# Kernel tuning notes

Hardware: AMD Instinct MI355X
Metric: run time of the kernel (lower is better)

Reference implementation:

```python
import jax, jax.numpy as jnp
import numpy as np

EMBED = 1024
DFF = 4096


def _layernorm(x, g, b, eps=1e-5):
    mu = jnp.mean(x, axis=-1, keepdims=True)
    var = jnp.var(x, axis=-1, keepdims=True)
    return (x - mu) * jax.lax.rsqrt(var + eps) * g + b


def setup_inputs() -> dict:
    key = jax.random.key(0)
    ks = jax.random.split(key, 14)
    s = 1.0 / np.sqrt(EMBED)
    sf = 1.0 / np.sqrt(DFF)
    d = {
        "src": jax.random.normal(ks[0], (4, 2048, EMBED), dtype=jnp.float32),
        "Wq": jax.random.uniform(ks[1], (EMBED, EMBED), jnp.float32, -s, s),
        "bq": jnp.zeros((EMBED,), jnp.float32),
        "Wk": jax.random.uniform(ks[2], (EMBED, EMBED), jnp.float32, -s, s),
        "bk": jnp.zeros((EMBED,), jnp.float32),
        "Wv": jax.random.uniform(ks[3], (EMBED, EMBED), jnp.float32, -s, s),
        "bv": jnp.zeros((EMBED,), jnp.float32),
        "Wo": jax.random.uniform(ks[4], (EMBED, EMBED), jnp.float32, -s, s),
        "bo": jnp.zeros((EMBED,), jnp.float32),
        "W1": jax.random.uniform(ks[5], (EMBED, DFF), jnp.float32, -s, s),
        "b1": jnp.zeros((DFF,), jnp.float32),
        "W2": jax.random.uniform(ks[6], (DFF, EMBED), jnp.float32, -sf, sf),
        "b2": jnp.zeros((EMBED,), jnp.float32),
        "g1": jnp.ones((EMBED,), jnp.float32),
        "be1": jnp.zeros((EMBED,), jnp.float32),
        "g2": jnp.ones((EMBED,), jnp.float32),
        "be2": jnp.zeros((EMBED,), jnp.float32),
    }
    return d


def reference(src, Wq, bq, Wk, bk, Wv, bv, Wo, bo, W1, b1, W2, b2, g1, be1, g2, be2):
    # Q/K/V projections: [b, s, d]
    Q = src @ Wq + bq
    K = src @ Wk + bk
    V = src @ Wv + bv
    # Single-head, UNSCALED attention (faithful to source: no 1/sqrt(d), num_heads unused)
    scores = jnp.einsum("bqd,bkd->bqk", Q, K)  # [b, s, s]
    weights = jax.nn.softmax(scores, axis=-1)
    attn = jnp.einsum("bqk,bkd->bqd", weights, V)
    attn = attn @ Wo + bo
    x = _layernorm(src + attn, g1, be1)
    ff = jax.nn.relu(x @ W1 + b1) @ W2 + b2
    return _layernorm(x + ff, g2, be2)
```

## Files before the change

### kernel.cpp

```cpp
#include <hip/hip_runtime.h>
#include <stdint.h>

typedef unsigned short u16;
typedef _Float16 v8h __attribute__((ext_vector_type(8)));
typedef float v4f __attribute__((ext_vector_type(4)));

static __device__ __forceinline__ float h2f(u16 u) {
    union { u16 s; _Float16 h; } v; v.s = u; return (float)v.h;
}
static __device__ __forceinline__ u16 f2h(float f) {
    union { u16 s; _Float16 h; } v; v.h = (_Float16)f; return v.s;
}

static __device__ __forceinline__ void gload_lds16(const u16* g, const u16* l) {
    __builtin_amdgcn_global_load_lds(
        (const __attribute__((address_space(1))) uint32_t*)(uintptr_t)g,
        (__attribute__((address_space(3))) uint32_t*)(uintptr_t)l,
        16, 0, 0);
}

__global__ __launch_bounds__(256) void cvt_f16(const float* __restrict__ in,
                                               u16* __restrict__ out, int n8) {
    const int i = blockIdx.x * 256 + threadIdx.x;
    if (i >= n8) return;
    const float4 a = ((const float4*)in)[2 * i];
    const float4 b = ((const float4*)in)[2 * i + 1];
    u16 o[8] = {f2h(a.x), f2h(a.y), f2h(a.z), f2h(a.w),
                f2h(b.x), f2h(b.y), f2h(b.z), f2h(b.w)};
    *(uint4*)(out + (size_t)i * 8) = *(const uint4*)o;
}

__global__ __launch_bounds__(256) void transpose_all(
    const float* __restrict__ Wq, const float* __restrict__ Wk,
    const float* __restrict__ Wv, const float* __restrict__ Wo,
    const float* __restrict__ W1, const float* __restrict__ W2,
    u16* __restrict__ WqkvT, u16* __restrict__ WoT,
    u16* __restrict__ W1T, u16* __restrict__ W2T)
{
    int t = blockIdx.x;
    const float* in; u16* out; long ldi, ldo; int xt;
    if (t < 1024)      {            in = Wq; out = WqkvT;               ldi = 1024; ldo = 1024; xt = 32; }
    else if (t < 2048) { t -= 1024; in = Wk; out = WqkvT + 1024*1024;   ldi = 1024; ldo = 1024; xt = 32; }
    else if (t < 3072) { t -= 2048; in = Wv; out = WqkvT + 2*1024*1024; ldi = 1024; ldo = 1024; xt = 32; }
    else if (t < 4096) { t -= 3072; in = Wo; out = WoT;                 ldi = 1024; ldo = 1024; xt = 32; }
    else if (t < 8192) { t -= 4096; in = W1; out = W1T;                 ldi = 4096; ldo = 1024; xt = 128; }
    else               { t -= 8192; in = W2; out = W2T;                 ldi = 1024; ldo = 4096; xt = 32; }
    const int c0 = (t % xt) * 32, r0 = (t / xt) * 32;
    __shared__ float tile[32][33];
    for (int i = threadIdx.y; i < 32; i += 8)
        tile[i][threadIdx.x] = in[(long)(r0 + i) * ldi + c0 + threadIdx.x];
    __syncthreads();
    for (int i = threadIdx.y; i < 32; i += 8)
        out[(long)(c0 + i) * ldo + r0 + threadIdx.x] = f2h(tile[threadIdx.x][i]);
}

template<int OMODE, int BIAS, bool RELU, int NX, int NY, int NZ>
__global__ __launch_bounds__(512) void gemm256(
    const u16* __restrict__ A, long lda, long Asb,
    const u16* __restrict__ B, long ldb, long Bsb,
    void* __restrict__ Cv, long ldc, long Csb, u16* __restrict__ C1,
    const float* __restrict__ bias, const float* __restrict__ bias2,
    const float* __restrict__ bias3, int K)
{
    constexpr int NWG = NX * NY * NZ;
    static_assert(NWG % 8 == 0, "XCD swizzle needs nwg % 8 == 0");
    alignas(16) __shared__ u16 As[4 * 8192];
    alignas(16) __shared__ u16 Bs[4 * 8192];

    const int tid = threadIdx.x;
    const int lane = tid & 63, wave = tid >> 6;
    const int l16 = lane & 15, quad = lane >> 4;
    const int wm = wave >> 2;
    const int wn = wave & 3;

    const int lin = blockIdx.x;
    const int tl = (lin & 7) * (NWG / 8) + (lin >> 3);
    const int xe = tl % NX;
    const int ye = (tl / NX) % NY;
    const int zb = tl / (NX * NY);
    const long m0 = (long)ye * 256;
    const long n0 = (long)xe * 256;

    const u16* Aop = A + (long)zb * Asb;
    const u16* Bop = B + (long)zb * Bsb;

    const int srow = tid >> 2;
    const int sq = (tid & 3) ^ ((tid >> 3) & 3);
    const long gaofs0 = (m0 + srow) * lda + sq * 8;
    const long gaofs1 = gaofs0 + 128 * lda;
    const long gbofs0 = (n0 + srow) * ldb + sq * 8;
    const long gbofs1 = gbofs0 + 128 * ldb;
    const int wv512n = wave * 512;

    const int swzE = (quad ^ ((l16 >> 1) & 3)) * 8;
    const int aRow = (wm * 128 + l16) * 32 + swzE;
    const int bRow = (wn * 64 + l16) * 32 + swzE;

    v4f acc[8][4];
#pragma unroll
    for (int i = 0; i < 8; ++i)
#pragma unroll
        for (int j = 0; j < 4; ++j)
            acc[i][j] = (v4f){0.f, 0.f, 0.f, 0.f};
    v8h bf[4];

#define STAGE_A(RIDX, KP) do { \
        u16* lb_ = As + (RIDX) * 8192 + wv512n; \
        gload_lds16(Aop + gaofs0 + (KP), lb_); \
        gload_lds16(Aop + gaofs1 + (KP), lb_ + 4096); } while (0)
#define STAGE_B(RIDX, KP) do { \
        u16* lb_ = Bs + (RIDX) * 8192 + wv512n; \
        gload_lds16(Bop + gbofs0 + (KP), lb_); \
        gload_lds16(Bop + gbofs1 + (KP), lb_ + 4096); } while (0)

#define MF(CH, I, J) \
    acc[(CH) * 4 + (I)][J] = __builtin_amdgcn_mfma_f32_16x16x32_f16( \
        af##I, bf[J], acc[(CH) * 4 + (I)][J], 0, 0, 0)

#define PHASE(BUF, KH, CH, EVENW, ...) { \
        if (EVENW) asm volatile("s_waitcnt vmcnt(6)" ::: "memory"); \
        const u16* Ar_ = As + ((BUF) * 2 + (KH)) * 8192 + aRow + (CH) * 2048; \
        v8h af0 = *(const v8h*)(Ar_); \
        v8h af1 = *(const v8h*)(Ar_ + 512); \
        v8h af2 = *(const v8h*)(Ar_ + 1024); \
        v8h af3 = *(const v8h*)(Ar_ + 1536); \
        if ((CH) == 0) { \
            const u16* Br_ = Bs + ((BUF) * 2 + (KH)) * 8192 + bRow; \
            bf[0] = *(const v8h*)(Br_); \
            bf[1] = *(const v8h*)(Br_ + 512); \
            bf[2] = *(const v8h*)(Br_ + 1024); \
            bf[3] = *(const v8h*)(Br_ + 1536); \
        } \
        __VA_ARGS__; \
        __builtin_amdgcn_s_barrier(); \
        asm volatile("s_waitcnt lgkmcnt(0)" ::: "memory"); \
        __builtin_amdgcn_s_setprio(1); \
        MF(CH,0,0); MF(CH,0,1); MF(CH,0,2); MF(CH,0,3); \
        MF(CH,1,0); MF(CH,1,1); MF(CH,1,2); MF(CH,1,3); \
        MF(CH,2,0); MF(CH,2,1); MF(CH,2,2); MF(CH,2,3); \
        MF(CH,3,0); MF(CH,3,1); MF(CH,3,2); MF(CH,3,3); \
        __builtin_amdgcn_s_setprio(0); \
        __builtin_amdgcn_s_barrier(); \
    }

    STAGE_A(0, 0);  STAGE_B(0, 0);
    STAGE_A(1, 32); STAGE_B(1, 32);
    STAGE_A(2, 64); STAGE_B(2, 64);
    asm volatile("s_waitcnt vmcnt(8)" ::: "memory");
    __builtin_amdgcn_s_barrier();

    const int NT = K >> 7;
#pragma unroll 1
    for (int t = 0; t < NT; ++t) {
        const long kb = (long)t * 128;
        const long kp1 = kb + 96;
        long kp2  = kb + 128; if (kp2  >= K) kp2  = 0;
        long kp2b = kb + 160; if (kp2b >= K) kp2b = 0;
        long kp3  = kb + 192; if (kp3  >= K) kp3  = 0;

        PHASE(0, 0, 0, false, STAGE_A(3, kp1))
        PHASE(0, 0, 1, true,  STAGE_B(3, kp1))
        PHASE(0, 1, 0, false, STAGE_A(0, kp2))
        PHASE(0, 1, 1, true,  STAGE_B(0, kp2))
        PHASE(1, 0, 0, false, STAGE_A(1, kp2b))
        PHASE(1, 0, 1, true,  STAGE_B(1, kp2b))
        PHASE(1, 1, 0, false, STAGE_A(2, kp3))
        PHASE(1, 1, 1, true,  STAGE_B(2, kp3))
    }

#undef PHASE
#undef MF
#undef STAGE_A
#undef STAGE_B

    float bv[4];
#pragma unroll
    for (int j = 0; j < 4; ++j) {
        const long col = n0 + wn * 64 + j * 16 + l16;
        if (BIAS == 0) bv[j] = 0.f;
        else if (BIAS == 1) bv[j] = bias[col];
        else {
            const int sel = (int)(col >> 10);
            const float* bp = sel == 0 ? bias : (sel == 1 ? bias2 : bias3);
            bv[j] = bp[col & 1023];
        }
    }

    if (OMODE == 3 && n0 >= 2048) {
        const long bb = m0 >> 11, mb = m0 & 2047;
        u16* C = C1 + bb * Csb;
#pragma unroll
        for (int j = 0; j < 4; ++j) {
            const long col = n0 - 2048 + wn * 64 + j * 16 + l16;
            u16* pc = C + col * 2048 + mb + wm * 128 + quad * 4;
#pragma unroll
            for (int i = 0; i < 8; ++i) {
                u16 o[4];
#pragma unroll
                for (int r = 0; r < 4; ++r) {
                    float val = acc[i][j][r] + bv[j];
                    if (RELU) val = fmaxf(val, 0.f);
                    o[r] = f2h(val);
                }
                *(uint2*)(pc + i * 16) = *(const uint2*)o;
            }
        }
    } else {
        const long cb = (OMODE == 3 ? 0 : (long)zb * Csb)
                      + (m0 + wm * 128 + quad * 4) * ldc + (n0 + wn * 64 + l16);
        u16* p0 = (u16*)Cv + cb;
#pragma unroll
        for (int i = 0; i < 8; ++i)
#pragma unroll
            for (int r = 0; r < 4; ++r) {
                u16* prow = p0 + (long)(i * 16 + r) * ldc;
#pragma unroll
                for (int j = 0; j < 4; ++j) {
                    float val = acc[i][j][r] + bv[j];
                    if (RELU) val = fmaxf(val, 0.f);
                    prow[j * 16] = f2h(val);
                }
            }
    }
}

template<int OMODE, int BIAS, bool RELU, int NX, int NY, int NZ>
__global__ __launch_bounds__(512) void gemm256n(
    const u16* __restrict__ A, long lda, long Asb,
    const u16* __restrict__ B, long ldb, long Bsb,
    void* __restrict__ Cv, long ldc, long Csb, u16* __restrict__ C1,
    const float* __restrict__ bias, const float* __restrict__ bias2,
    const float* __restrict__ bias3, int K)
{
    constexpr int NWG = NX * NY * NZ;
    static_assert(NWG % 8 == 0, "XCD swizzle needs nwg % 8 == 0");
    alignas(16) __shared__ u16 As[4 * 8192];
    alignas(16) __shared__ u16 Bs[4 * 4096];

    const int tid = threadIdx.x;
    const int lane = tid & 63, wave = tid >> 6;
    const int l16 = lane & 15, quad = lane >> 4;
    const int wm = wave >> 2;
    const int wn = wave & 3;

    const int lin = blockIdx.x;
    const int tl = (lin & 7) * (NWG / 8) + (lin >> 3);
    const int xe = tl % NX;
    const int ye = (tl / NX) % NY;
    const int zb = tl / (NX * NY);
    const long m0 = (long)ye * 256;
    const long n0 = (long)xe * 128;

    const u16* Aop = A + (long)zb * Asb;
    const u16* Bop = B + (long)zb * Bsb;

    const int srow = tid >> 2;
    const int sq = (tid & 3) ^ ((tid >> 3) & 3);
    const long gaofs0 = (m0 + srow) * lda + sq * 8;
    const long gaofs1 = gaofs0 + 128 * lda;
    const long gbofs0 = (n0 + srow) * ldb + sq * 8;
    const int wv512n = wave * 512;

    const int swzE = (quad ^ ((l16 >> 1) & 3)) * 8;
    const int aRow = (wm * 128 + l16) * 32 + swzE;
    const int bRow = (wn * 32 + l16) * 32 + swzE;

    v4f acc[8][2];
#pragma unroll
    for (int i = 0; i < 8; ++i)
#pragma unroll
        for (int j = 0; j < 2; ++j)
            acc[i][j] = (v4f){0.f, 0.f, 0.f, 0.f};
    v8h bf[2];

#define STAGE_A(RIDX, KP) do { \
        u16* lb_ = As + (RIDX) * 8192 + wv512n; \
        gload_lds16(Aop + gaofs0 + (KP), lb_); \
        gload_lds16(Aop + gaofs1 + (KP), lb_ + 4096); } while (0)
#define STAGE_B(RIDX, KP) do { \
        gload_lds16(Bop + gbofs0 + (KP), Bs + (RIDX) * 4096 + wv512n); } while (0)

#define MF(CH, I, J) \
    acc[(CH) * 4 + (I)][J] = __builtin_amdgcn_mfma_f32_16x16x32_f16( \
        af##I, bf[J], acc[(CH) * 4 + (I)][J], 0, 0, 0)

#define PHASE(BUF, KH, CH, EVENW, ...) { \
        if (EVENW) asm volatile("s_waitcnt vmcnt(5)" ::: "memory"); \
        const u16* Ar_ = As + ((BUF) * 2 + (KH)) * 8192 + aRow + (CH) * 2048; \
        v8h af0 = *(const v8h*)(Ar_); \
        v8h af1 = *(const v8h*)(Ar_ + 512); \
        v8h af2 = *(const v8h*)(Ar_ + 1024); \
        v8h af3 = *(const v8h*)(Ar_ + 1536); \
        if ((CH) == 0) { \
            const u16* Br_ = Bs + ((BUF) * 2 + (KH)) * 4096 + bRow; \
            bf[0] = *(const v8h*)(Br_); \
            bf[1] = *(const v8h*)(Br_ + 512); \
        } \
        __VA_ARGS__; \
        __builtin_amdgcn_s_barrier(); \
        asm volatile("s_waitcnt lgkmcnt(0)" ::: "memory"); \
        __builtin_amdgcn_s_setprio(1); \
        MF(CH,0,0); MF(CH,0,1); \
        MF(CH,1,0); MF(CH,1,1); \
        MF(CH,2,0); MF(CH,2,1); \
        MF(CH,3,0); MF(CH,3,1); \
        __builtin_amdgcn_s_setprio(0); \
        __builtin_amdgcn_s_barrier(); \
    }

    STAGE_A(0, 0);  STAGE_B(0, 0);
    STAGE_A(1, 32); STAGE_B(1, 32);
    STAGE_A(2, 64); STAGE_B(2, 64);
    asm volatile("s_waitcnt vmcnt(6)" ::: "memory");
    __builtin_amdgcn_s_barrier();

    const int NT = K >> 7;
#pragma unroll 1
    for (int t = 0; t < NT; ++t) {
        const long kb = (long)t * 128;
        const long kp1 = kb + 96;
        long kp2  = kb + 128; if (kp2  >= K) kp2  = 0;
        long kp2b = kb + 160; if (kp2b >= K) kp2b = 0;
        long kp3  = kb + 192; if (kp3  >= K) kp3  = 0;

        PHASE(0, 0, 0, false, STAGE_A(3, kp1))
        PHASE(0, 0, 1, true,  STAGE_B(3, kp1))
        PHASE(0, 1, 0, false, STAGE_A(0, kp2))
        PHASE(0, 1, 1, true,  STAGE_B(0, kp2))
        PHASE(1, 0, 0, false, STAGE_A(1, kp2b))
        PHASE(1, 0, 1, true,  STAGE_B(1, kp2b))
        PHASE(1, 1, 0, false, STAGE_A(2, kp3))
        PHASE(1, 1, 1, true,  STAGE_B(2, kp3))
    }

#undef PHASE
#undef MF
#undef STAGE_A
#undef STAGE_B

    float bv[2];
#pragma unroll
    for (int j = 0; j < 2; ++j) {
        const long col = n0 + wn * 32 + j * 16 + l16;
        if (BIAS == 0) bv[j] = 0.f;
        else if (BIAS == 1) bv[j] = bias[col];
        else {
            const int sel = (int)(col >> 10);
            const float* bp = sel == 0 ? bias : (sel == 1 ? bias2 : bias3);
            bv[j] = bp[col & 1023];
        }
    }

    if (OMODE == 3 && n0 >= 2048) {
        const long bb = m0 >> 11, mb = m0 & 2047;
        u16* C = C1 + bb * Csb;
#pragma unroll
        for (int j = 0; j < 2; ++j) {
            const long col = n0 - 2048 + wn * 32 + j * 16 + l16;
            u16* pc = C + col * 2048 + mb + wm * 128 + quad * 4;
#pragma unroll
            for (int i = 0; i < 8; ++i) {
                u16 o[4];
#pragma unroll
                for (int r = 0; r < 4; ++r) {
                    float val = acc[i][j][r] + bv[j];
                    if (RELU) val = fmaxf(val, 0.f);
                    o[r] = f2h(val);
                }
                *(uint2*)(pc + i * 16) = *(const uint2*)o;
            }
        }
    } else {
        const long cb = (OMODE == 3 ? 0 : (long)zb * Csb)
                      + (m0 + wm * 128 + quad * 4) * ldc + (n0 + wn * 32 + l16);
        u16* p0 = (u16*)Cv + cb;
#pragma unroll
        for (int i = 0; i < 8; ++i)
#pragma unroll
            for (int r = 0; r < 4; ++r) {
                u16* prow = p0 + (long)(i * 16 + r) * ldc;
#pragma unroll
                for (int j = 0; j < 2; ++j) {
                    float val = acc[i][j][r] + bv[j];
                    if (RELU) val = fmaxf(val, 0.f);
                    prow[j * 16] = f2h(val);
                }
            }
    }
}

__global__ __launch_bounds__(256) void softmax_rows(u16* __restrict__ S) {
    const long row = blockIdx.x;
    u16* p = S + row * 2048;
    const int t = threadIdx.x;
    float v[8];
    float mx = -1e30f;
#pragma unroll
    for (int i = 0; i < 8; ++i) { v[i] = h2f(p[t + i * 256]); mx = fmaxf(mx, v[i]); }
    __shared__ float red[256];
    red[t] = mx; __syncthreads();
    for (int off = 128; off > 0; off >>= 1) {
        if (t < off) red[t] = fmaxf(red[t], red[t + off]);
        __syncthreads();
    }
    mx = red[0]; __syncthreads();
    float sum = 0.f;
#pragma unroll
    for (int i = 0; i < 8; ++i) { v[i] = __expf(v[i] - mx); sum += v[i]; }
    red[t] = sum; __syncthreads();
    for (int off = 128; off > 0; off >>= 1) {
        if (t < off) red[t] += red[t + off];
        __syncthreads();
    }
    const float inv = 1.f / red[0];
#pragma unroll
    for (int i = 0; i < 8; ++i) p[t + i * 256] = f2h(v[i] * inv);
}

__global__ __launch_bounds__(256) void ln_one(
    const float* __restrict__ a, const u16* __restrict__ bb,
    const float* __restrict__ g, const float* __restrict__ be,
    u16* __restrict__ out16)
{
    const long base = (long)blockIdx.x * 1024;
    const int t = threadIdx.x;
    float v[4]; float s = 0.f, ss = 0.f;
#pragma unroll
    for (int i = 0; i < 4; ++i) {
        const int c = t + i * 256;
        const float x = a[base + c] + h2f(bb[base + c]);
        v[i] = x; s += x; ss += x * x;
    }
    __shared__ float rs[256], rss[256];
    rs[t] = s; rss[t] = ss; __syncthreads();
    for (int off = 128; off > 0; off >>= 1) {
        if (t < off) { rs[t] += rs[t + off]; rss[t] += rss[t + off]; }
        __syncthreads();
    }
    const float mean = rs[0] * (1.f / 1024.f);
    const float var = rss[0] * (1.f / 1024.f) - mean * mean;
    const float rstd = rsqrtf(var + 1e-5f);
#pragma unroll
    for (int i = 0; i < 4; ++i) {
        const int c = t + i * 256;
        out16[base + c] = f2h((v[i] - mean) * rstd * g[c] + be[c]);
    }
}

__global__ __launch_bounds__(256) void ln_two(
    const u16* __restrict__ a, const u16* __restrict__ bb,
    const float* __restrict__ g, const float* __restrict__ be,
    float* __restrict__ out)
{
    const long base = (long)blockIdx.x * 1024;
    const int t = threadIdx.x;
    float v[4]; float s = 0.f, ss = 0.f;
#pragma unroll
    for (int i = 0; i < 4; ++i) {
        const int c = t + i * 256;
        const float x = h2f(a[base + c]) + h2f(bb[base + c]);
        v[i] = x; s += x; ss += x * x;
    }
    __shared__ float rs[256], rss[256];
    rs[t] = s; rss[t] = ss; __syncthreads();
    for (int off = 128; off > 0; off >>= 1) {
        if (t < off) { rs[t] += rs[t + off]; rss[t] += rss[t + off]; }
        __syncthreads();
    }
    const float mean = rs[0] * (1.f / 1024.f);
    const float var = rss[0] * (1.f / 1024.f) - mean * mean;
    const float rstd = rsqrtf(var + 1e-5f);
#pragma unroll
    for (int i = 0; i < 4; ++i) {
        const int c = t + i * 256;
        out[base + c] = (v[i] - mean) * rstd * g[c] + be[c];
    }
}

extern "C" void kernel_launch(void* const* d_in, const int* in_sizes, int n_in,
                              void* d_out, int out_size, void* d_ws, size_t ws_size,
                              hipStream_t stream) {
    (void)in_sizes; (void)n_in; (void)out_size; (void)ws_size;
    constexpr long S = 2048, E = 1024, F = 4096, M = 8192;

    const float* src = (const float*)d_in[0];
    const float* Wq  = (const float*)d_in[1];
    const float* bq  = (const float*)d_in[2];
    const float* Wk  = (const float*)d_in[3];
    const float* bk  = (const float*)d_in[4];
    const float* Wv  = (const float*)d_in[5];
    const float* bv  = (const float*)d_in[6];
    const float* Wo  = (const float*)d_in[7];
    const float* bo  = (const float*)d_in[8];
    const float* W1  = (const float*)d_in[9];
    const float* b1  = (const float*)d_in[10];
    const float* W2  = (const float*)d_in[11];
    const float* b2  = (const float*)d_in[12];
    const float* g1  = (const float*)d_in[13];
    const float* be1 = (const float*)d_in[14];
    const float* g2  = (const float*)d_in[15];
    const float* be2 = (const float*)d_in[16];

    char* ws = (char*)d_ws;
    size_t off = 0;
    auto take = [&](size_t bytes) {
        char* p = ws + off;
        off += (bytes + 255) & ~(size_t)255;
        return p;
    };
    const size_t MB16 = 16777216;
    u16*   srcH  = (u16*)take(MB16);
    u16*   WqkvT = (u16*)take(3 * E * E * 2);
    u16*   WoT   = (u16*)take(E * E * 2);
    u16*   W1T   = (u16*)take(F * E * 2);
    u16*   W2T   = (u16*)take(E * F * 2);
    char*  B0    = take(2 * MB16);
    char*  B1    = take(MB16);
    char*  B2    = take(4ull * S * S * 4);
    char*  B3    = take(MB16);
    char*  B4    = take(MB16);

    u16*   QK    = (u16*)B0;
    u16*   VT    = (u16*)B1;
    u16*   Sh    = (u16*)B2;
    u16*   hf    = (u16*)B2;
    u16*   attn  = (u16*)B3;
    u16*   xh    = (u16*)B3;
    u16*   attnO = (u16*)B4;
    u16*   ffO   = (u16*)B4;

    dim3 blk(256), blk5(512), tb(32, 8);

    cvt_f16<<<dim3(M * E / 8 / 256), blk, 0, stream>>>(src, srcH, M * E / 8);

    transpose_all<<<dim3(12288), tb, 0, stream>>>(Wq, Wk, Wv, Wo, W1, W2,
                                                  WqkvT, WoT, W1T, W2T);

    gemm256n<3, 3, false, 24, 32, 1><<<dim3(24 * 32), blk5, 0, stream>>>(
        srcH, E, 0, WqkvT, E, 0, QK, 2 * E, E * S, VT, bq, bk, bv, E);

    gemm256<0, 0, false, 8, 8, 4><<<dim3(8 * 8 * 4), blk5, 0, stream>>>(
        QK, 2 * E, S * 2 * E, QK + E, 2 * E, S * 2 * E,
        Sh, S, S * S, nullptr, nullptr, nullptr, nullptr, E);

    softmax_rows<<<dim3(M), blk, 0, stream>>>(Sh);

    gemm256n<0, 0, false, 8, 8, 4><<<dim3(8 * 8 * 4), blk5, 0, stream>>>(
        Sh, S, S * S, VT, S, E * S,
        attn, E, S * E, nullptr, nullptr, nullptr, nullptr, S);

    gemm256n<0, 1, false, 8, 32, 1><<<dim3(8 * 32), blk5, 0, stream>>>(
        attn, E, 0, WoT, E, 0, attnO, E, 0, nullptr, bo, nullptr, nullptr, E);

    ln_one<<<dim3(M), blk, 0, stream>>>(src, attnO, g1, be1, xh);

    gemm256<0, 1, true, 16, 32, 1><<<dim3(16 * 32), blk5, 0, stream>>>(
        xh, E, 0, W1T, E, 0, hf, F, 0, nullptr, b1, nullptr, nullptr, E);

    gemm256n<0, 1, false, 8, 32, 1><<<dim3(8 * 32), blk5, 0, stream>>>(
        hf, F, 0, W2T, F, 0, ffO, E, 0, nullptr, b2, nullptr, nullptr, F);

    ln_two<<<dim3(M), blk, 0, stream>>>(xh, ffO, g2, be2, (float*)d_out);
}
```

Before: 508.6 us.

## Software-pipeline LDS fragment loads under MFMAs in the large GEMM kernel

```diff
diff --git a/kernel.cpp b/kernel.cpp
--- a/kernel.cpp
+++ b/kernel.cpp
@@ -102,7 +102,8 @@
 #pragma unroll
         for (int j = 0; j < 4; ++j)
             acc[i][j] = (v4f){0.f, 0.f, 0.f, 0.f};
-    v8h bf[4];
+    v8h af[4];
+    v8h bfr[2][4];
 
 #define STAGE_A(RIDX, KP) do { \
         u16* lb_ = As + (RIDX) * 8192 + wv512n; \
@@ -113,33 +114,33 @@
         gload_lds16(Bop + gbofs0 + (KP), lb_); \
         gload_lds16(Bop + gbofs1 + (KP), lb_ + 4096); } while (0)
 
-#define MF(CH, I, J) \
-    acc[(CH) * 4 + (I)][J] = __builtin_amdgcn_mfma_f32_16x16x32_f16( \
-        af##I, bf[J], acc[(CH) * 4 + (I)][J], 0, 0, 0)
-
-#define PHASE(BUF, KH, CH, EVENW, ...) { \
-        if (EVENW) asm volatile("s_waitcnt vmcnt(6)" ::: "memory"); \
-        const u16* Ar_ = As + ((BUF) * 2 + (KH)) * 8192 + aRow + (CH) * 2048; \
-        v8h af0 = *(const v8h*)(Ar_); \
-        v8h af1 = *(const v8h*)(Ar_ + 512); \
-        v8h af2 = *(const v8h*)(Ar_ + 1024); \
-        v8h af3 = *(const v8h*)(Ar_ + 1536); \
-        if ((CH) == 0) { \
-            const u16* Br_ = Bs + ((BUF) * 2 + (KH)) * 8192 + bRow; \
-            bf[0] = *(const v8h*)(Br_); \
-            bf[1] = *(const v8h*)(Br_ + 512); \
-            bf[2] = *(const v8h*)(Br_ + 1024); \
-            bf[3] = *(const v8h*)(Br_ + 1536); \
-        } \
-        __VA_ARGS__; \
-        __builtin_amdgcn_s_barrier(); \
-        asm volatile("s_waitcnt lgkmcnt(0)" ::: "memory"); \
+#define MF4(CH, I, BC) \
+    acc[(CH)*4+(I)][0] = __builtin_amdgcn_mfma_f32_16x16x32_f16(af[I], bfr[BC][0], acc[(CH)*4+(I)][0], 0, 0, 0); \
+    acc[(CH)*4+(I)][1] = __builtin_amdgcn_mfma_f32_16x16x32_f16(af[I], bfr[BC][1], acc[(CH)*4+(I)][1], 0, 0, 0); \
+    acc[(CH)*4+(I)][2] = __builtin_amdgcn_mfma_f32_16x16x32_f16(af[I], bfr[BC][2], acc[(CH)*4+(I)][2], 0, 0, 0); \
+    acc[(CH)*4+(I)][3] = __builtin_amdgcn_mfma_f32_16x16x32_f16(af[I], bfr[BC][3], acc[(CH)*4+(I)][3], 0, 0, 0);
+
+#define PHASE(CH, BC, NRD, NCH, BLN, BN, ODD, STG) { \
+        STG; \
         __builtin_amdgcn_s_setprio(1); \
-        MF(CH,0,0); MF(CH,0,1); MF(CH,0,2); MF(CH,0,3); \
-        MF(CH,1,0); MF(CH,1,1); MF(CH,1,2); MF(CH,1,3); \
-        MF(CH,2,0); MF(CH,2,1); MF(CH,2,2); MF(CH,2,3); \
-        MF(CH,3,0); MF(CH,3,1); MF(CH,3,2); MF(CH,3,3); \
+        MF4(CH, 0, BC) \
+        MF4(CH, 1, BC) \
+        { const u16* Ar_ = As + (NRD) * 8192 + aRow + (NCH) * 2048; \
+          af[0] = *(const v8h*)(Ar_); \
+          af[1] = *(const v8h*)(Ar_ + 512); \
+          if (BLN) { const u16* Br_ = Bs + (NRD) * 8192 + bRow; \
+            bfr[BN][0] = *(const v8h*)(Br_); \
+            bfr[BN][1] = *(const v8h*)(Br_ + 512); \
+            bfr[BN][2] = *(const v8h*)(Br_ + 1024); \
+            bfr[BN][3] = *(const v8h*)(Br_ + 1536); } } \
+        MF4(CH, 2, BC) \
+        { const u16* Ar_ = As + (NRD) * 8192 + aRow + (NCH) * 2048; \
+          af[2] = *(const v8h*)(Ar_ + 1024); } \
+        MF4(CH, 3, BC) \
+        { const u16* Ar_ = As + (NRD) * 8192 + aRow + (NCH) * 2048; \
+          af[3] = *(const v8h*)(Ar_ + 1536); } \
         __builtin_amdgcn_s_setprio(0); \
+        if (ODD) asm volatile("s_waitcnt vmcnt(6)" ::: "memory"); \
         __builtin_amdgcn_s_barrier(); \
     }
 
@@ -148,6 +149,11 @@
     STAGE_A(2, 64); STAGE_B(2, 64);
     asm volatile("s_waitcnt vmcnt(8)" ::: "memory");
     __builtin_amdgcn_s_barrier();
+
+#pragma unroll
+    for (int i = 0; i < 4; ++i) af[i] = *(const v8h*)&As[aRow + i * 512];
+#pragma unroll
+    for (int j = 0; j < 4; ++j) bfr[0][j] = *(const v8h*)&Bs[bRow + j * 512];
 
     const int NT = K >> 7;
 #pragma unroll 1
@@ -158,18 +164,21 @@
         long kp2b = kb + 160; if (kp2b >= K) kp2b = 0;
         long kp3  = kb + 192; if (kp3  >= K) kp3  = 0;
 
-        PHASE(0, 0, 0, false, STAGE_A(3, kp1))
-        PHASE(0, 0, 1, true,  STAGE_B(3, kp1))
-        PHASE(0, 1, 0, false, STAGE_A(0, kp2))
-        PHASE(0, 1, 1, true,  STAGE_B(0, kp2))
-        PHASE(1, 0, 0, false, STAGE_A(1, kp2b))
-        PHASE(1, 0, 1, true,  STAGE_B(1, kp2b))
-        PHASE(1, 1, 0, false, STAGE_A(2, kp3))
-        PHASE(1, 1, 1, true,  STAGE_B(2, kp3))
-    }
+        PHASE(0, 0,  0,  1,  0, 0, 1, STAGE_A(3, kp1))
+        PHASE(1, 0,  1,  0,  1, 1, 0, STAGE_B(3, kp1))
+        PHASE(0, 1,  1,  1,  0, 0, 1, STAGE_A(0, kp2))
+        PHASE(1, 1,  2,  0,  1, 0, 0, STAGE_B(0, kp2))
+        PHASE(0, 0,  2,  1,  0, 0, 1, STAGE_A(1, kp2b))
+        PHASE(1, 0,  3,  0,  1, 1, 0, STAGE_B(1, kp2b))
+        PHASE(0, 1,  3,  1,  0, 0, 1, STAGE_A(2, kp3))
+        PHASE(1, 1,  0,  0,  1, 0, 0, STAGE_B(2, kp3))
+    }
+
+    asm volatile("s_waitcnt vmcnt(0) lgkmcnt(0)" ::: "memory");
+    __builtin_amdgcn_s_barrier();
 
 #undef PHASE
-#undef MF
+#undef MF4
 #undef STAGE_A
 #undef STAGE_B
 
@@ -280,17 +289,18 @@
 #define STAGE_B(RIDX, KP) do { \
         gload_lds16(Bop + gbofs0 + (KP), Bs + (RIDX) * 4096 + wv512n); } while (0)
 
-#define MF(CH, I, J) \
-    acc[(CH) * 4 + (I)][J] = __builtin_amdgcn_mfma_f32_16x16x32_f16( \
-        af##I, bf[J], acc[(CH) * 4 + (I)][J], 0, 0, 0)
+#define MF2(CH, I) \
+    acc[(CH) * 4 + (I)][0] = __builtin_amdgcn_mfma_f32_16x16x32_f16(af[I], bf[0], acc[(CH) * 4 + (I)][0], 0, 0, 0); \
+    acc[(CH) * 4 + (I)][1] = __builtin_amdgcn_mfma_f32_16x16x32_f16(af[I], bf[1], acc[(CH) * 4 + (I)][1], 0, 0, 0);
 
 #define PHASE(BUF, KH, CH, EVENW, ...) { \
         if (EVENW) asm volatile("s_waitcnt vmcnt(5)" ::: "memory"); \
         const u16* Ar_ = As + ((BUF) * 2 + (KH)) * 8192 + aRow + (CH) * 2048; \
-        v8h af0 = *(const v8h*)(Ar_); \
-        v8h af1 = *(const v8h*)(Ar_ + 512); \
-        v8h af2 = *(const v8h*)(Ar_ + 1024); \
-        v8h af3 = *(const v8h*)(Ar_ + 1536); \
+        v8h af[4]; \
+        af[0] = *(const v8h*)(Ar_); \
+        af[1] = *(const v8h*)(Ar_ + 512); \
+        af[2] = *(const v8h*)(Ar_ + 1024); \
+        af[3] = *(const v8h*)(Ar_ + 1536); \
         if ((CH) == 0) { \
             const u16* Br_ = Bs + ((BUF) * 2 + (KH)) * 4096 + bRow; \
             bf[0] = *(const v8h*)(Br_); \
@@ -300,10 +310,10 @@
         __builtin_amdgcn_s_barrier(); \
         asm volatile("s_waitcnt lgkmcnt(0)" ::: "memory"); \
         __builtin_amdgcn_s_setprio(1); \
-        MF(CH,0,0); MF(CH,0,1); \
-        MF(CH,1,0); MF(CH,1,1); \
-        MF(CH,2,0); MF(CH,2,1); \
-        MF(CH,3,0); MF(CH,3,1); \
+        MF2(CH, 0) \
+        MF2(CH, 1) \
+        MF2(CH, 2) \
+        MF2(CH, 3) \
         __builtin_amdgcn_s_setprio(0); \
         __builtin_amdgcn_s_barrier(); \
     }
@@ -334,7 +344,7 @@
     }
 
 #undef PHASE
-#undef MF
+#undef MF2
 #undef STAGE_A
 #undef STAGE_B
 
```

After: 504.5 us. No clear change (-0.8%).
